# Optimization experiments

Hardware: AMD Instinct MI355X
Metric: run time of the kernel (lower is better)

The kernel has to match this reference:

```python
import jax, jax.numpy as jnp
import numpy as np

N = 200000      # hits
K = 64          # max objects (t_idx values 1..64; 0 = noise)
NCC = 2         # n_ccoords
NCLS = 6        # n_classes
Q_MIN = 0.1
S_B = 1.0
E_DEN_OFF = 1.0  # energy_den_offset


def huber(x, d):
    absx = jnp.abs(x)
    return jnp.where(absx < d, x * x, d * d + 2.0 * d * (absx - d))


def softclip(x, s):
    y = x / s
    y = jnp.where(y > 1.0, jnp.log(y + 1.0), y)
    return y * s


def div_no_nan(a, b):
    return jnp.where(b == 0.0, 0.0, a / jnp.where(b == 0.0, 1.0, b))


def setup_inputs() -> dict:
    key = jax.random.key(0)
    ks = jax.random.split(key, 10)
    return {
        'beta': jax.random.uniform(ks[0], (N, 1), jnp.float32, 1e-3, 1.0 - 1e-3),
        'ccoords': jax.random.normal(ks[1], (N, NCC), jnp.float32),
        'pred_energy': jax.random.uniform(ks[2], (N, 1), jnp.float32) * 50.0,
        'pred_pos': jax.random.normal(ks[3], (N, NCC), jnp.float32),
        'pred_time': jax.random.normal(ks[4], (N, 1), jnp.float32),
        'pred_id': jax.random.normal(ks[5], (N, NCLS), jnp.float32),
        't_energy': jax.random.uniform(ks[6], (N, 1), jnp.float32) * 50.0,
        't_pos': jax.random.normal(ks[7], (N, NCC), jnp.float32),
        't_time': jax.random.normal(ks[8], (N, 1), jnp.float32),
        't_idx': jax.random.randint(ks[9], (N, 1), 0, K + 1, jnp.int32),
    }


def oc_loss(beta, ccoords, pred_energy, pred_pos, pred_time, pred_id,
            t_energy, t_pos, t_time, t_idx):
    tidx = t_idx[:, 0]                                   # [N]
    M = jax.nn.one_hot(tidx, K + 1, dtype=beta.dtype)[:, 1:]   # [N,K], obj ids 1..K
    is_noise = (tidx == 0).astype(beta.dtype)            # [N]

    b = jnp.clip(beta[:, 0], 1e-6, 1.0 - 1e-6)           # [N]
    q = jnp.arctanh(b) ** 2 + Q_MIN                      # [N] charge

    # condensation point (alpha) per object: highest-beta hit of the object
    padded_b = jnp.where(M > 0, b[:, None], -1.0)        # [N,K]
    alpha = jnp.argmax(padded_b, axis=0)                 # [K]
    n_per_obj = jnp.sum(M, axis=0)                       # [K]
    valid = (n_per_obj > 0).astype(b.dtype)              # [K]
    n_valid = jnp.maximum(jnp.sum(valid), 1.0)

    x_alpha = ccoords[alpha]                             # [K,C]
    q_alpha = q[alpha]                                   # [K]
    b_alpha = b[alpha]                                   # [K]

    # pairwise hit <-> condensation point distances
    diff = ccoords[:, None, :] - x_alpha[None, :, :]     # [N,K,C]
    d2 = jnp.sum(diff * diff, axis=-1)                   # [N,K]
    d = jnp.sqrt(d2 + 1e-9)

    qq = q[:, None] * q_alpha[None, :]                   # [N,K]
    Nf = jnp.asarray(N, b.dtype)

    # attractive potential (hits of the object), normalized by total hits
    att_k = jnp.sum(qq * d2 * M, axis=0) / Nf            # [K]
    L_att = jnp.sum(att_k * valid) / n_valid

    # repulsive potential (hits NOT of the object, incl. noise)
    rep_k = jnp.sum(qq * jax.nn.relu(1.0 - d) * (1.0 - M), axis=0) / Nf
    L_rep = jnp.sum(rep_k * valid) / n_valid

    # beta loss: sharpen condensation points + suppress noise beta
    n_noise = jnp.maximum(jnp.sum(is_noise), 1.0)
    L_beta = (jnp.sum((1.0 - b_alpha) * valid) / n_valid
              + S_B * jnp.sum(b * is_noise) / n_noise)

    # ---- payload losses (per-hit, beta-weighted per object) ----
    # energy weights (calc_energy_weights)
    te = t_energy[:, 0]
    w_e = jax.nn.relu(jnp.where(te > 10.0, 1.0, (te - 0.5) / 10.0 * 10.0 / 9.5))

    # energy loss (default branch of calc_energy_loss)
    eloss = softclip(div_no_nan((te - pred_energy[:, 0]) ** 2, te + E_DEN_OFF), 10.0)
    # position loss (calc_position_loss)
    dp2 = jnp.sum((t_pos - pred_pos) ** 2, axis=-1)      # [N]
    ploss = softclip(huber(jnp.sqrt(dp2 / 100.0 + 0.01), 10.0), 3.0)
    # timing loss (calc_timing_loss)
    tloss = softclip(huber(t_time[:, 0] - pred_time[:, 0], 2.0), 6.0)
    # classification loss (calc_classification_loss)
    closs = 1e-8 * jnp.mean(pred_id ** 2, axis=-1)       # [N]

    pw = M * b[:, None]                                  # payload weights [N,K]
    pw_den = jnp.sum(pw, axis=0) + 1e-9                  # [K]

    def payload(loss_per_hit):
        num = jnp.sum(pw * (loss_per_hit * w_e)[:, None], axis=0)  # [K]
        return jnp.sum((num / pw_den) * valid) / n_valid

    L_E = payload(eloss)
    L_pos = payload(ploss)
    L_t = payload(tloss)
    L_cls = payload(closs)

    # all loss weights / scalings are 1.0 per init_kwargs
    return L_att + L_rep + L_beta + L_E + L_pos + L_t + L_cls


def reference(beta, ccoords, pred_energy, pred_pos, pred_time, pred_id,
              t_energy, t_pos, t_time, t_idx):
    return oc_loss(beta, ccoords, pred_energy, pred_pos, pred_time, pred_id,
                   t_energy, t_pos, t_time, t_idx)
```

## Files before the change

kernel.cpp:

```cpp
#include <hip/hip_runtime.h>
#include <math.h>

typedef unsigned long long ull;
#define NOBJ 64
#define GA 256
#define TA 512
#define GB 256
#define TB 512

__device__ __forceinline__ float clipb(float b) {
    return fminf(fmaxf(b, 1e-6f), 1.0f - 1e-6f);
}
__device__ __forceinline__ float huber_f(float x, float d) {
    float ax = fabsf(x);
    return ax < d ? x * x : d * d + 2.0f * d * (ax - d);
}
__device__ __forceinline__ float softclip_f(float x, float s) {
    float y = x * (1.0f / s);
    y = y > 1.0f ? __logf(y + 1.0f) : y;
    return y * s;
}
__device__ __forceinline__ float atanh_sq_q(float b) {
    float a = 0.5f * __logf(__fdividef(1.0f + b, 1.0f - b));
    return a * a + 0.1f;
}


__global__ __launch_bounds__(TA) void pass_a(
    const float* __restrict__ beta, const int* __restrict__ tidx, int n,
    ull* __restrict__ keysG, float* __restrict__ denG, int* __restrict__ noiseG,
    float* __restrict__ out)
{
    __shared__ ull skey[NOBJ];
    __shared__ float sden[NOBJ];
    __shared__ int snoise;
    const int t = threadIdx.x, bid = blockIdx.x;

    if (t < NOBJ) { skey[t] = 0ull; sden[t] = 0.0f; }
    if (t == 0) snoise = 0;
    __syncthreads();

    for (int i = bid * TA + t; i < n; i += GA * TA) {
        int ti = tidx[i];
        float b = clipb(beta[i]);
        if (ti > 0) {
            int k = ti - 1;
            ull key = ((ull)__float_as_uint(b) << 32) |
                      (ull)(0xFFFFFFFFu - (unsigned)i);
            atomicMax(&skey[k], key);
            atomicAdd(&sden[k], b);
        } else {
            atomicAdd(&snoise, 1);
        }
    }
    __syncthreads();

    if (t < NOBJ) {
        if (skey[t])          atomicMax(&keysG[t], skey[t]);
        if (sden[t] != 0.0f)  atomicAdd(&denG[t], sden[t]);
    }
    if (t == 0) {
        if (snoise) atomicAdd(noiseG, snoise);
        if (bid == 0) out[0] = 0.0f;
    }
}

__global__ __launch_bounds__(TB) void pass_b(
    const float* __restrict__ beta, const float* __restrict__ cc,
    const float* __restrict__ pe, const float* __restrict__ pp,
    const float* __restrict__ pt,
    const float* __restrict__ te, const float* __restrict__ tp,
    const float* __restrict__ tt, const int* __restrict__ tidx,
    int n, float invN,
    const ull* __restrict__ keysG, const float* __restrict__ denG,
    const int* __restrict__ noiseG, float* __restrict__ out)
{
    __shared__ float4 kc[NOBJ];
    __shared__ float sc[3];
    __shared__ float swf[TB / 64];
    const int t = threadIdx.x, bid = blockIdx.x;

    if (t < NOBJ) {
        ull key = keysG[t];
        bool valid = (key != 0ull);
        unsigned idx = 0xFFFFFFFFu - (unsigned)(key & 0xFFFFFFFFull);
        int alpha = valid ? (int)idx : 0;
        float ba = valid ? __uint_as_float((unsigned)(key >> 32)) : 0.5f;
        float qa = atanh_sq_q(ba);
        float2 ca = *(const float2*)(cc + 2 * alpha);
        float4 c4;
        c4.x = ca.x;
        c4.y = ca.y;
        c4.z = valid ? qa : 0.0f;
        c4.w = valid ? __fdividef(1.0f, denG[t] + 1e-9f) : 0.0f;
        kc[t] = c4;

        float v  = valid ? 1.0f : 0.0f;
        float bs = valid ? (1.0f - ba) : 0.0f;
        for (int off = 32; off >= 1; off >>= 1) {
            v  += __shfl_down(v, off);
            bs += __shfl_down(bs, off);
        }
        if (t == 0) {
            float nv = fmaxf(v, 1.0f);
            sc[0] = 1.0f / nv;
            sc[1] = 1.0f / fmaxf((float)noiseG[0], 1.0f);
            sc[2] = bs / nv;
        }
    }
    __syncthreads();
    const float inv_nvalid  = sc[0];
    const float noise_scale = sc[1];

    float acc = 0.0f;
    for (int i = bid * TB + t; i < n; i += GB * TB) {
        int ti = tidx[i];
        int own = ti - 1;
        float b = clipb(beta[i]);
        float q = atanh_sq_q(b);
        float2 ci = *(const float2*)(cc + 2 * i);

        float geo = 0.0f;
        #pragma unroll 8
        for (int k = 0; k < NOBJ; ++k) {
            float4 c4 = kc[k];
            float dx = ci.x - c4.x;
            float dy = ci.y - c4.y;
            float d2 = dx * dx + dy * dy;
            float rep = fmaxf(1.0f - sqrtf(d2 + 1e-9f), 0.0f);
            float term = (k == own) ? d2 : rep;
            geo += c4.z * term;
        }
        float loss_i = q * geo * invN;

        if (own >= 0) {
            float tev = te[i];
            float we = fmaxf(tev > 10.0f ? 1.0f : (tev - 0.5f) * (1.0f / 9.5f), 0.0f);
            float diff = tev - pe[i];
            float el = softclip_f(__fdividef(diff * diff, tev + 1.0f), 10.0f);

            float2 tpv = *(const float2*)(tp + 2 * i);
            float2 ppv = *(const float2*)(pp + 2 * i);
            float dpx = tpv.x - ppv.x;
            float dpy = tpv.y - ppv.y;
            float dp2 = dpx * dpx + dpy * dpy;
            float pl = softclip_f(huber_f(sqrtf(dp2 * 0.01f + 0.01f), 10.0f), 3.0f);

            float tl = softclip_f(huber_f(tt[i] - pt[i], 2.0f), 6.0f);

            loss_i += b * we * (el + pl + tl) * kc[own].w;
            loss_i *= inv_nvalid;
        } else {
            loss_i *= inv_nvalid;
            loss_i += b * noise_scale;
        }
        acc += loss_i;
    }

    for (int off = 32; off >= 1; off >>= 1) acc += __shfl_down(acc, off);
    if ((t & 63) == 0) swf[t >> 6] = acc;
    __syncthreads();
    if (t == 0) {
        float s = 0.0f;
        #pragma unroll
        for (int w = 0; w < TB / 64; ++w) s += swf[w];
        if (bid == 0) s += sc[2];
        atomicAdd(out, s);
    }
}

extern "C" void kernel_launch(void* const* d_in, const int* in_sizes, int n_in,
                              void* d_out, int out_size, void* d_ws, size_t ws_size,
                              hipStream_t stream) {
    const float* beta = (const float*)d_in[0];
    const float* cc   = (const float*)d_in[1];
    const float* pe   = (const float*)d_in[2];
    const float* pp   = (const float*)d_in[3];
    const float* pt   = (const float*)d_in[4];
    const float* te   = (const float*)d_in[6];
    const float* tp   = (const float*)d_in[7];
    const float* tt   = (const float*)d_in[8];
    const int*   tidx = (const int*)d_in[9];
    int n = in_sizes[0];

    char* ws = (char*)d_ws;
    ull*   keysG  = (ull*)(ws + 0);
    float* denG   = (float*)(ws + 512);
    int*   noiseG = (int*)(ws + 768);
    float* out    = (float*)d_out;

    float invN = 1.0f / (float)n;
    hipMemsetAsync(d_ws, 0, 1024, stream);
    pass_a<<<GA, TA, 0, stream>>>(beta, tidx, n, keysG, denG, noiseG, out);
    pass_b<<<GB, TB, 0, stream>>>(beta, cc, pe, pp, pt, te, tp, tt, tidx,
                                  n, invN, keysG, denG, noiseG, out);
}
```

Before: 103.3 us.

## Fuse two passes into one cooperative kernel with grid-sync reductions

Merges the per-object argmax/denominator pass and the loss pass into a single cooperative kernel. Global atomics are replaced by per-block partials in workspace, reduced by dedicated blocks between two grid.sync barriers. This removes the memset and the second launch. The inner 64-object loop also drops the per-k owner select by correcting the owner term afterwards, and the unroll factor goes up. The grid-wide barriers add their own cost, and a cooperative launch needs all 256 blocks to be resident at once.

```diff
diff --git a/kernel.cpp b/kernel.cpp
--- a/kernel.cpp
+++ b/kernel.cpp
@@ -1,12 +1,13 @@
 #include <hip/hip_runtime.h>
+#include <hip/hip_cooperative_groups.h>
 #include <math.h>
+
+namespace cg = cooperative_groups;
 
 typedef unsigned long long ull;
 #define NOBJ 64
-#define GA 256
-#define TA 512
-#define GB 256
-#define TB 512
+#define G 256
+#define T 512
 
 __device__ __forceinline__ float clipb(float b) {
     return fminf(fmaxf(b, 1e-6f), 1.0f - 1e-6f);
@@ -26,21 +27,35 @@
 }
 
 
-__global__ __launch_bounds__(TA) void pass_a(
-    const float* __restrict__ beta, const int* __restrict__ tidx, int n,
-    ull* __restrict__ keysG, float* __restrict__ denG, int* __restrict__ noiseG,
-    float* __restrict__ out)
+__global__ __launch_bounds__(T) void oc_fused(
+    const float* __restrict__ beta, const float* __restrict__ cc,
+    const float* __restrict__ pe, const float* __restrict__ pp,
+    const float* __restrict__ pt,
+    const float* __restrict__ te, const float* __restrict__ tp,
+    const float* __restrict__ tt, const int* __restrict__ tidx,
+    int n, float invN,
+    ull* __restrict__ partsK, float* __restrict__ partsD,
+    int* __restrict__ partsN,
+    float4* __restrict__ kcG, float2* __restrict__ auxG,
+    float* __restrict__ nzG, float* __restrict__ out)
 {
-    __shared__ ull skey[NOBJ];
+    cg::grid_group grid = cg::this_grid();
+    __shared__ ull   skey[NOBJ];
     __shared__ float sden[NOBJ];
-    __shared__ int snoise;
+    __shared__ int   snoise;
+    __shared__ float4 kc[NOBJ];
+    __shared__ float sc[3];
+    __shared__ ull   wk[T / 64];
+    __shared__ float wd[T / 64];
+    __shared__ float swf[T / 64];
+
     const int t = threadIdx.x, bid = blockIdx.x;
 
     if (t < NOBJ) { skey[t] = 0ull; sden[t] = 0.0f; }
     if (t == 0) snoise = 0;
     __syncthreads();
 
-    for (int i = bid * TA + t; i < n; i += GA * TA) {
+    for (int i = bid * T + t; i < n; i += G * T) {
         int ti = tidx[i];
         float b = clipb(beta[i]);
         if (ti > 0) {
@@ -54,49 +69,68 @@
         }
     }
     __syncthreads();
-
     if (t < NOBJ) {
-        if (skey[t])          atomicMax(&keysG[t], skey[t]);
-        if (sden[t] != 0.0f)  atomicAdd(&denG[t], sden[t]);
+        partsK[t * G + bid] = skey[t];
+        partsD[t * G + bid] = sden[t];
     }
     if (t == 0) {
-        if (snoise) atomicAdd(noiseG, snoise);
+        partsN[bid] = snoise;
         if (bid == 0) out[0] = 0.0f;
     }
-}
-
-__global__ __launch_bounds__(TB) void pass_b(
-    const float* __restrict__ beta, const float* __restrict__ cc,
-    const float* __restrict__ pe, const float* __restrict__ pp,
-    const float* __restrict__ pt,
-    const float* __restrict__ te, const float* __restrict__ tp,
-    const float* __restrict__ tt, const int* __restrict__ tidx,
-    int n, float invN,
-    const ull* __restrict__ keysG, const float* __restrict__ denG,
-    const int* __restrict__ noiseG, float* __restrict__ out)
-{
-    __shared__ float4 kc[NOBJ];
-    __shared__ float sc[3];
-    __shared__ float swf[TB / 64];
-    const int t = threadIdx.x, bid = blockIdx.x;
+    grid.sync();
+
+    if (bid < NOBJ) {
+        ull mk = 0ull; float sd = 0.0f;
+        if (t < G) {
+            mk = partsK[bid * G + t];
+            sd = partsD[bid * G + t];
+        }
+        for (int off = 32; off >= 1; off >>= 1) {
+            ull o = __shfl_down(mk, off);
+            mk = o > mk ? o : mk;
+            sd += __shfl_down(sd, off);
+        }
+        if ((t & 63) == 0) { wk[t >> 6] = mk; wd[t >> 6] = sd; }
+        __syncthreads();
+        if (t == 0) {
+            #pragma unroll
+            for (int w = 1; w < T / 64; ++w) {
+                mk = wk[w] > mk ? wk[w] : mk;
+                sd += wd[w];
+            }
+            bool valid = (mk != 0ull);
+            unsigned idx = 0xFFFFFFFFu - (unsigned)(mk & 0xFFFFFFFFull);
+            int alpha = valid ? (int)idx : 0;
+            float ba = valid ? __uint_as_float((unsigned)(mk >> 32)) : 0.5f;
+            float qa = atanh_sq_q(ba);
+            float2 ca = *(const float2*)(cc + 2 * alpha);
+            float4 c4;
+            c4.x = ca.x;
+            c4.y = ca.y;
+            c4.z = valid ? qa : 0.0f;
+            c4.w = valid ? __fdividef(1.0f, sd + 1e-9f) : 0.0f;
+            kcG[bid] = c4;
+            auxG[bid] = make_float2(valid ? 1.0f : 0.0f,
+                                    valid ? (1.0f - ba) : 0.0f);
+        }
+    } else if (bid == NOBJ) {
+        float nz = (t < G) ? (float)partsN[t] : 0.0f;
+        for (int off = 32; off >= 1; off >>= 1) nz += __shfl_down(nz, off);
+        if ((t & 63) == 0) wd[t >> 6] = nz;
+        __syncthreads();
+        if (t == 0) {
+            #pragma unroll
+            for (int w = 1; w < T / 64; ++w) nz += wd[w];
+            nzG[0] = nz;
+        }
+    }
+    grid.sync();
 
     if (t < NOBJ) {
-        ull key = keysG[t];
-        bool valid = (key != 0ull);
-        unsigned idx = 0xFFFFFFFFu - (unsigned)(key & 0xFFFFFFFFull);
-        int alpha = valid ? (int)idx : 0;
-        float ba = valid ? __uint_as_float((unsigned)(key >> 32)) : 0.5f;
-        float qa = atanh_sq_q(ba);
-        float2 ca = *(const float2*)(cc + 2 * alpha);
-        float4 c4;
-        c4.x = ca.x;
-        c4.y = ca.y;
-        c4.z = valid ? qa : 0.0f;
-        c4.w = valid ? __fdividef(1.0f, denG[t] + 1e-9f) : 0.0f;
+        float4 c4 = kcG[t];
         kc[t] = c4;
-
-        float v  = valid ? 1.0f : 0.0f;
-        float bs = valid ? (1.0f - ba) : 0.0f;
+        float2 ax = auxG[t];
+        float v = ax.x, bs = ax.y;
         for (int off = 32; off >= 1; off >>= 1) {
             v  += __shfl_down(v, off);
             bs += __shfl_down(bs, off);
@@ -104,16 +138,17 @@
         if (t == 0) {
             float nv = fmaxf(v, 1.0f);
             sc[0] = 1.0f / nv;
-            sc[1] = 1.0f / fmaxf((float)noiseG[0], 1.0f);
+            sc[1] = 1.0f / fmaxf(nzG[0], 1.0f);
             sc[2] = bs / nv;
         }
     }
     __syncthreads();
-    const float inv_nvalid  = sc[0];
+    const float inv_nv      = sc[0];
     const float noise_scale = sc[1];
+    const float qscale      = invN * inv_nv;
 
     float acc = 0.0f;
-    for (int i = bid * TB + t; i < n; i += GB * TB) {
+    for (int i = bid * T + t; i < n; i += G * T) {
         int ti = tidx[i];
         int own = ti - 1;
         float b = clipb(beta[i]);
@@ -121,19 +156,25 @@
         float2 ci = *(const float2*)(cc + 2 * i);
 
         float geo = 0.0f;
-        #pragma unroll 8
+        #pragma unroll 16
         for (int k = 0; k < NOBJ; ++k) {
             float4 c4 = kc[k];
             float dx = ci.x - c4.x;
             float dy = ci.y - c4.y;
-            float d2 = dx * dx + dy * dy;
+            float d2 = fmaf(dx, dx, dy * dy);
             float rep = fmaxf(1.0f - sqrtf(d2 + 1e-9f), 0.0f);
-            float term = (k == own) ? d2 : rep;
-            geo += c4.z * term;
-        }
-        float loss_i = q * geo * invN;
-
+            geo = fmaf(c4.z, rep, geo);
+        }
+
+        float extra;
         if (own >= 0) {
+            float4 co = kc[own];
+            float dx = ci.x - co.x;
+            float dy = ci.y - co.y;
+            float d2 = fmaf(dx, dx, dy * dy);
+            float rep = fmaxf(1.0f - sqrtf(d2 + 1e-9f), 0.0f);
+            geo = fmaf(co.z, d2 - rep, geo);
+
             float tev = te[i];
             float we = fmaxf(tev > 10.0f ? 1.0f : (tev - 0.5f) * (1.0f / 9.5f), 0.0f);
             float diff = tev - pe[i];
@@ -143,18 +184,15 @@
             float2 ppv = *(const float2*)(pp + 2 * i);
             float dpx = tpv.x - ppv.x;
             float dpy = tpv.y - ppv.y;
-            float dp2 = dpx * dpx + dpy * dpy;
-            float pl = softclip_f(huber_f(sqrtf(dp2 * 0.01f + 0.01f), 10.0f), 3.0f);
+            float pl = softclip_f(huber_f(sqrtf(fmaf(dpx, dpx, dpy * dpy) * 0.01f + 0.01f), 10.0f), 3.0f);
 
             float tl = softclip_f(huber_f(tt[i] - pt[i], 2.0f), 6.0f);
 
-            loss_i += b * we * (el + pl + tl) * kc[own].w;
-            loss_i *= inv_nvalid;
+            extra = b * we * (el + pl + tl) * co.w * inv_nv;
         } else {
-            loss_i *= inv_nvalid;
-            loss_i += b * noise_scale;
-        }
-        acc += loss_i;
+            extra = b * noise_scale;
+        }
+        acc += fmaf(q * geo, qscale, extra);
     }
 
     for (int off = 32; off >= 1; off >>= 1) acc += __shfl_down(acc, off);
@@ -163,7 +201,7 @@
     if (t == 0) {
         float s = 0.0f;
         #pragma unroll
-        for (int w = 0; w < TB / 64; ++w) s += swf[w];
+        for (int w = 0; w < T / 64; ++w) s += swf[w];
         if (bid == 0) s += sc[2];
         atomicAdd(out, s);
     }
@@ -182,16 +220,19 @@
     const float* tt   = (const float*)d_in[8];
     const int*   tidx = (const int*)d_in[9];
     int n = in_sizes[0];
+    float invN = 1.0f / (float)n;
 
     char* ws = (char*)d_ws;
-    ull*   keysG  = (ull*)(ws + 0);
-    float* denG   = (float*)(ws + 512);
-    int*   noiseG = (int*)(ws + 768);
-    float* out    = (float*)d_out;
-
-    float invN = 1.0f / (float)n;
-    hipMemsetAsync(d_ws, 0, 1024, stream);
-    pass_a<<<GA, TA, 0, stream>>>(beta, tidx, n, keysG, denG, noiseG, out);
-    pass_b<<<GB, TB, 0, stream>>>(beta, cc, pe, pp, pt, te, tp, tt, tidx,
-                                  n, invN, keysG, denG, noiseG, out);
-}
+    ull*    partsK = (ull*)(ws + 0);
+    float*  partsD = (float*)(ws + 131072);
+    int*    partsN = (int*)(ws + 196608);
+    float4* kcG    = (float4*)(ws + 197632);
+    float2* auxG   = (float2*)(ws + 198656);
+    float*  nzG    = (float*)(ws + 199168);
+    float*  out    = (float*)d_out;
+
+    void* args[] = { &beta, &cc, &pe, &pp, &pt, &te, &tp, &tt, &tidx,
+                     &n, &invN, &partsK, &partsD, &partsN, &kcG, &auxG,
+                     &nzG, &out };
+    hipLaunchCooperativeKernel((void*)oc_fused, dim3(G), dim3(T), args, 0, stream);
+}
```

Measured after the change: 176.2 us. 1.71x slower.

## Use one-element-per-thread grids and hoist own-object term out of inner loop

Applied to the files above, without the earlier changes.

pass_b now launches enough 256-thread blocks to cover every hit once, instead of running a grid-stride loop over a fixed 256-block grid. All per-hit loads are issued up front. The per-k select between attractive and repulsive terms is removed: the inner loop always accumulates the repulsive term, and a single correction for the hit's own object is added afterwards. pass_a handles two hits per thread with int2/float2 vector loads and no stride loop, so it only covers all hits when n is at most 2*GA*TA. That size limit is silently assumed.

```diff
diff --git a/kernel.cpp b/kernel.cpp
--- a/kernel.cpp
+++ b/kernel.cpp
@@ -5,8 +5,7 @@
 #define NOBJ 64
 #define GA 256
 #define TA 512
-#define GB 256
-#define TB 512
+#define TB 256
 
 __device__ __forceinline__ float clipb(float b) {
     return fminf(fmaxf(b, 1e-6f), 1.0f - 1e-6f);
@@ -40,17 +39,39 @@
     if (t == 0) snoise = 0;
     __syncthreads();
 
-    for (int i = bid * TA + t; i < n; i += GA * TA) {
-        int ti = tidx[i];
-        float b = clipb(beta[i]);
-        if (ti > 0) {
-            int k = ti - 1;
-            ull key = ((ull)__float_as_uint(b) << 32) |
-                      (ull)(0xFFFFFFFFu - (unsigned)i);
-            atomicMax(&skey[k], key);
-            atomicAdd(&sden[k], b);
+    const int j = bid * TA + t;
+    const int i0 = 2 * j;
+    if (i0 < n) {
+        int2 tv;  float2 bv;
+        const bool has1 = (i0 + 1 < n);
+        if (has1) {
+            tv = ((const int2*)tidx)[j];
+            bv = ((const float2*)beta)[j];
         } else {
-            atomicAdd(&snoise, 1);
+            tv.x = tidx[i0]; tv.y = 0;
+            bv.x = beta[i0]; bv.y = 0.0f;
+        }
+        {
+            float b = clipb(bv.x);
+            if (tv.x > 0) {
+                ull key = ((ull)__float_as_uint(b) << 32) |
+                          (ull)(0xFFFFFFFFu - (unsigned)i0);
+                atomicMax(&skey[tv.x - 1], key);
+                atomicAdd(&sden[tv.x - 1], b);
+            } else {
+                atomicAdd(&snoise, 1);
+            }
+        }
+        if (has1) {
+            float b = clipb(bv.y);
+            if (tv.y > 0) {
+                ull key = ((ull)__float_as_uint(b) << 32) |
+                          (ull)(0xFFFFFFFFu - (unsigned)(i0 + 1));
+                atomicMax(&skey[tv.y - 1], key);
+                atomicAdd(&sden[tv.y - 1], b);
+            } else {
+                atomicAdd(&snoise, 1);
+            }
         }
     }
     __syncthreads();
@@ -109,52 +130,61 @@
         }
     }
     __syncthreads();
-    const float inv_nvalid  = sc[0];
+    const float inv_nv      = sc[0];
     const float noise_scale = sc[1];
+    const float qscale      = invN * inv_nv;
 
     float acc = 0.0f;
-    for (int i = bid * TB + t; i < n; i += GB * TB) {
-        int ti = tidx[i];
+    const int i = bid * TB + t;
+    if (i < n) {
+        int ti       = tidx[i];
+        float b      = clipb(beta[i]);
+        float2 ci    = *(const float2*)(cc + 2 * i);
+        float tev    = te[i];
+        float pev    = pe[i];
+        float2 tpv   = *(const float2*)(tp + 2 * i);
+        float2 ppv   = *(const float2*)(pp + 2 * i);
+        float ttv    = tt[i];
+        float ptv    = pt[i];
+
         int own = ti - 1;
-        float b = clipb(beta[i]);
         float q = atanh_sq_q(b);
-        float2 ci = *(const float2*)(cc + 2 * i);
 
         float geo = 0.0f;
-        #pragma unroll 8
+        #pragma unroll 16
         for (int k = 0; k < NOBJ; ++k) {
             float4 c4 = kc[k];
             float dx = ci.x - c4.x;
             float dy = ci.y - c4.y;
-            float d2 = dx * dx + dy * dy;
+            float d2 = fmaf(dx, dx, dy * dy);
             float rep = fmaxf(1.0f - sqrtf(d2 + 1e-9f), 0.0f);
-            float term = (k == own) ? d2 : rep;
-            geo += c4.z * term;
-        }
-        float loss_i = q * geo * invN;
-
+            geo = fmaf(c4.z, rep, geo);
+        }
+
+        float extra;
         if (own >= 0) {
-            float tev = te[i];
+            float4 co = kc[own];
+            float dx = ci.x - co.x;
+            float dy = ci.y - co.y;
+            float d2 = fmaf(dx, dx, dy * dy);
+            float rep = fmaxf(1.0f - sqrtf(d2 + 1e-9f), 0.0f);
+            geo = fmaf(co.z, d2 - rep, geo);
+
             float we = fmaxf(tev > 10.0f ? 1.0f : (tev - 0.5f) * (1.0f / 9.5f), 0.0f);
-            float diff = tev - pe[i];
+            float diff = tev - pev;
             float el = softclip_f(__fdividef(diff * diff, tev + 1.0f), 10.0f);
 
-            float2 tpv = *(const float2*)(tp + 2 * i);
-            float2 ppv = *(const float2*)(pp + 2 * i);
             float dpx = tpv.x - ppv.x;
             float dpy = tpv.y - ppv.y;
-            float dp2 = dpx * dpx + dpy * dpy;
-            float pl = softclip_f(huber_f(sqrtf(dp2 * 0.01f + 0.01f), 10.0f), 3.0f);
-
-            float tl = softclip_f(huber_f(tt[i] - pt[i], 2.0f), 6.0f);
-
-            loss_i += b * we * (el + pl + tl) * kc[own].w;
-            loss_i *= inv_nvalid;
+            float pl = softclip_f(huber_f(sqrtf(fmaf(dpx, dpx, dpy * dpy) * 0.01f + 0.01f), 10.0f), 3.0f);
+
+            float tl = softclip_f(huber_f(ttv - ptv, 2.0f), 6.0f);
+
+            extra = b * we * (el + pl + tl) * co.w * inv_nv;
         } else {
-            loss_i *= inv_nvalid;
-            loss_i += b * noise_scale;
-        }
-        acc += loss_i;
+            extra = b * noise_scale;
+        }
+        acc = fmaf(q * geo, qscale, extra);
     }
 
     for (int off = 32; off >= 1; off >>= 1) acc += __shfl_down(acc, off);
@@ -190,6 +220,7 @@
     float* out    = (float*)d_out;
 
     float invN = 1.0f / (float)n;
+    int GB = (n + TB - 1) / TB;
     hipMemsetAsync(d_ws, 0, 1024, stream);
     pass_a<<<GA, TA, 0, stream>>>(beta, tidx, n, keysG, denG, noiseG, out);
     pass_b<<<GB, TB, 0, stream>>>(beta, cc, pe, pp, pt, te, tp, tt, tidx,
```

New measurement: 102.4 us. No clear change (-0.9%).
